# Performance work log

Measured on AMD Instinct MI355X. Metric: run time of the kernel, lower is better.

The kernel has to match this reference:

```python
import jax, jax.numpy as jnp
import numpy as np

E, D_IN, H1, H2 = 10, 784, 256, 64


def setup_inputs() -> dict:
    key = jax.random.key(0)
    ks = jax.random.split(key, 11)
    s = lambda fan_in: 1.0 / np.sqrt(fan_in)
    return {
        "x": jax.random.normal(ks[0], (65536, D_IN), dtype=jnp.float32),
        # stacked expert weights (E experts of Linear layers)
        "W1": jax.random.uniform(ks[1], (E, D_IN, H1), jnp.float32, -s(D_IN), s(D_IN)),
        "b1": jax.random.uniform(ks[2], (E, H1), jnp.float32, -s(D_IN), s(D_IN)),
        "W2": jax.random.uniform(ks[3], (E, H1, H2), jnp.float32, -s(H1), s(H1)),
        "b2": jax.random.uniform(ks[4], (E, H2), jnp.float32, -s(H1), s(H1)),
        "W3": jax.random.uniform(ks[5], (E, H2), jnp.float32, -s(H2), s(H2)),  # [E,64,1] squeezed
        "b3": jax.random.uniform(ks[6], (E,), jnp.float32, -s(H2), s(H2)),
        # gate: 784 -> 256 -> E
        "Wg1": jax.random.uniform(ks[7], (D_IN, H1), jnp.float32, -s(D_IN), s(D_IN)),
        "bg1": jax.random.uniform(ks[8], (H1,), jnp.float32, -s(D_IN), s(D_IN)),
        "Wg2": jax.random.uniform(ks[9], (H1, E), jnp.float32, -s(H1), s(H1)),
        "bg2": jax.random.uniform(ks[10], (E,), jnp.float32, -s(H1), s(H1)),
    }


def reference(x, W1, b1, W2, b2, W3, b3, Wg1, bg1, Wg2, bg2):
    # dense all-experts MLP stack, batched over experts as grouped GEMMs
    h = jax.nn.relu(jnp.einsum("bi,eih->beh", x, W1) + b1)        # [B,E,256]
    h = jax.nn.relu(jnp.einsum("beh,ehk->bek", h, W2) + b2)        # [B,E,64]
    expert_outputs = jnp.einsum("bek,ek->be", h, W3) + b3          # [B,E]
    g = jax.nn.relu(x @ Wg1 + bg1)
    gate_scores = jax.nn.softmax(g @ Wg2 + bg2, axis=-1)           # [B,E]
    output = gate_scores * expert_outputs                          # [B,E]
    return (output, gate_scores, expert_outputs)
```

## Files before the change

### kernel.cpp

```cpp
#include <hip/hip_runtime.h>
#include <hip/hip_bf16.h>
#include <stdint.h>

#define BTOT   65536
#define DIN    784
#define K1P    800
#define NH1    256
#define NH2    64
#define NEXP   10
#define BM     64
#define NKS1   25
#define NKS2   9

#define XS_B      102400
#define H_OFF     XS_B
#define H_B       36864
#define EXP2_OFF  (H_OFF + H_B)
#define W3S_OFF   (EXP2_OFF + BM * NEXP * 2 * 4)
#define B3S_OFF   (W3S_OFF + NEXP * NH2 * 4)
#define LDS_TOTAL (B3S_OFF + 64)

typedef short s16x8  __attribute__((ext_vector_type(8)));
typedef float f32x4  __attribute__((ext_vector_type(4)));
typedef float f32x16 __attribute__((ext_vector_type(16)));

__device__ __forceinline__ short bf16b(float v) {
    __bf16 b = (__bf16)v;
    return __builtin_bit_cast(short, b);
}

__global__ void prep_w1(const float* __restrict__ W1, const float* __restrict__ b1,
                        const float* __restrict__ Wg1, const float* __restrict__ bg1,
                        __bf16* __restrict__ dst) {
    int t = blockIdx.x * 256 + threadIdx.x;
    int lane = t & 63;
    int rr = t >> 6;
    int kh = rr & 1;
    int ks = (rr >> 1) % 25;
    int nb = ((rr >> 1) / 25) % 8;
    int e  = (rr >> 1) / 200;
    int n  = nb * 32 + (lane & 31);
    int k0 = ks * 32 + kh * 16 + (lane >> 5) * 8;
    const float* src  = (e < NEXP) ? (W1 + (size_t)e * DIN * NH1) : Wg1;
    const float* bias = (e < NEXP) ? (b1 + e * NH1) : bg1;
    s16x8 o;
    #pragma unroll
    for (int j = 0; j < 8; ++j) {
        int k = k0 + j;
        float v = (k < DIN) ? src[(size_t)k * NH1 + n]
                            : ((k == DIN) ? bias[n] : 0.f);
        o[j] = bf16b(v);
    }
    *(s16x8*)((short*)dst + (size_t)t * 8) = o;
}

__global__ void prep_w2(const float* __restrict__ W2, const float* __restrict__ b2,
                        __bf16* __restrict__ dst) {
    int t = blockIdx.x * 256 + threadIdx.x;
    int lane = t & 63;
    int rr = t >> 6;
    int kh = rr & 1;
    int ks = (rr >> 1) % 9;
    int jb = ((rr >> 1) / 9) & 1;
    int e  = (rr >> 1) / 18;
    int n  = jb * 32 + (lane & 31);
    int k0 = ks * 32 + kh * 16 + (lane >> 5) * 8;
    s16x8 o;
    #pragma unroll
    for (int j = 0; j < 8; ++j) {
        int k = k0 + j;
        float v = (k < NH1) ? W2[((size_t)e * NH1 + k) * NH2 + n]
                            : ((k == NH1) ? b2[e * NH2 + n] : 0.f);
        o[j] = bf16b(v);
    }
    *(s16x8*)((short*)dst + (size_t)t * 8) = o;
}

__global__ void prep_wg2(const float* __restrict__ Wg2, const float* __restrict__ bg2,
                         __bf16* __restrict__ dst) {
    int t = blockIdx.x * 256 + threadIdx.x;
    if (t >= 9 * 2 * 64) return;
    int lane = t & 63;
    int rr = t >> 6;
    int kh = rr & 1;
    int ks = rr >> 1;
    int n  = lane & 31;
    int k0 = ks * 32 + kh * 16 + (lane >> 5) * 8;
    s16x8 o;
    #pragma unroll
    for (int j = 0; j < 8; ++j) {
        int k = k0 + j;
        float v = 0.f;
        if (n < NEXP) {
            if (k < NH1)       v = Wg2[(size_t)k * NEXP + n];
            else if (k == NH1) v = bg2[n];
        }
        o[j] = bf16b(v);
    }
    *(s16x8*)((short*)dst + (size_t)t * 8) = o;
}

#define PFA(S, T)                                                             \
    { _Pragma("unroll") for (int mt = 0; mt < 2; ++mt)                        \
        _Pragma("unroll") for (int kh = 0; kh < 2; ++kh)                      \
            a[S][mt][kh] = *(const s16x8*)(pA + ((mt * 25 + (T)) * 2 + kh) * 1024); }

#define PFW(S, E, T, PW)                                                      \
    { _Pragma("unroll") for (int nt = 0; nt < 2; ++nt)                        \
        _Pragma("unroll") for (int kh = 0; kh < 2; ++kh)                      \
            w[S][E][nt][kh] = *(const s16x8*)((PW) + nt * 51200                \
                                              + ((T) * 2 + kh) * 1024); }

#define PMMA(S, E)                                                            \
    { _Pragma("unroll") for (int nt = 0; nt < 2; ++nt)                        \
        _Pragma("unroll") for (int mt = 0; mt < 2; ++mt)                      \
            _Pragma("unroll") for (int kh = 0; kh < 2; ++kh)                  \
                acc[E][nt][mt] = __builtin_amdgcn_mfma_f32_32x32x16_bf16(     \
                    w[S][E][nt][kh], a[S][mt][kh], acc[E][nt][mt], 0, 0, 0); }

#define ZACC(E)                                                               \
    { _Pragma("unroll") for (int nt = 0; nt < 2; ++nt)                        \
        _Pragma("unroll") for (int mt = 0; mt < 2; ++mt)                      \
            _Pragma("unroll") for (int q = 0; q < 16; ++q)                    \
                acc[E][nt][mt][q] = 0.f; }

#define HWRITE(E)                                                             \
    { _Pragma("unroll") for (int mt = 0; mt < 2; ++mt)                        \
        _Pragma("unroll") for (int nt = 0; nt < 2; ++nt) {                    \
            const int ks2 = wave * 2 + nt;                                    \
            _Pragma("unroll") for (int q = 0; q < 4; ++q) {                   \
                uint2 wv; short* p = (short*)&wv;                             \
                _Pragma("unroll") for (int r2 = 0; r2 < 4; ++r2)              \
                    p[r2] = bf16b(fmaxf(acc[E][nt][mt][q * 4 + r2], 0.f));    \
                *(uint2*)(hb + ((mt * 9 + ks2) * 2 + (q >> 1)) * 1024         \
                             + (q & 1) * 512 + rl * 16 + hi * 8) = wv;        \
            } } }

#define PF_V2(PV)                                                             \
    { _Pragma("unroll") for (int p = 0; p < 3; ++p)                           \
        _Pragma("unroll") for (int kh = 0; kh < 2; ++kh)                      \
            v2[p][kh] = *(const s16x8*)((PV) + (p * 2 + kh) * 1024); }

#define L2_PF(S, T)                                                           \
    { _Pragma("unroll") for (int kh = 0; kh < 2; ++kh) {                      \
        hfr[S][kh] = *(const s16x8*)(pH + ((T) * 2 + kh) * 1024);             \
        v2[S][kh]  = *(const s16x8*)(pV + ((T) * 2 + kh) * 1024); } }

#define L2_MMA(S)                                                             \
    { _Pragma("unroll") for (int kh = 0; kh < 2; ++kh)                        \
        acc2 = __builtin_amdgcn_mfma_f32_32x32x16_bf16(                       \
            v2[S][kh], hfr[S][kh], acc2, 0, 0, 0); }

#define DO_L2(EV, PV)                                                         \
    {                                                                         \
        const char* pV = (PV);                                                \
        f32x16 acc2;                                                          \
        _Pragma("unroll") for (int q = 0; q < 16; ++q) acc2[q] = 0.f;         \
        _Pragma("unroll") for (int kh = 0; kh < 2; ++kh)                      \
            hfr[0][kh] = *(const s16x8*)(pH + (0 * 2 + kh) * 1024);           \
        _Pragma("unroll") for (int kh = 0; kh < 2; ++kh)                      \
            hfr[1][kh] = *(const s16x8*)(pH + (1 * 2 + kh) * 1024);           \
        _Pragma("unroll") for (int kh = 0; kh < 2; ++kh)                      \
            hfr[2][kh] = *(const s16x8*)(pH + (2 * 2 + kh) * 1024);           \
        _Pragma("unroll 1") for (int T = 0; T < 2; ++T) {                     \
            const int t3 = 3 * T;                                             \
            L2_MMA(0) L2_PF(0, t3 + 3)                                        \
            L2_MMA(1) L2_PF(1, t3 + 4)                                        \
            L2_MMA(2) L2_PF(2, t3 + 5)                                        \
        }                                                                     \
        L2_MMA(0) L2_MMA(1) L2_MMA(2)                                         \
        float part = 0.f;                                                     \
        const float* w3p = w3s + (EV) * NH2 + jb * 32 + 4 * hi;               \
        _Pragma("unroll") for (int q = 0; q < 4; ++q) {                       \
            f32x4 w3v = *(const f32x4*)(w3p + 8 * q);                         \
            _Pragma("unroll") for (int r2 = 0; r2 < 4; ++r2)                  \
                part += fmaxf(acc2[q * 4 + r2], 0.f) * w3v[r2];               \
        }                                                                     \
        part += __shfl_xor(part, 32, 64);                                     \
        if (hi == 0)                                                          \
            expl2[(mb2 * 32 + rl) * (NEXP * 2) + (EV) * 2 + jb] = part;       \
    }

__global__ void __launch_bounds__(256, 1)
moe_fused(const float* __restrict__ x, const float* __restrict__ W3,
          const float* __restrict__ b3, const __bf16* __restrict__ w1t,
          const __bf16* __restrict__ w2t, const __bf16* __restrict__ wg2t,
          float* __restrict__ out)
{
    extern __shared__ char lds[];
    char*  xsb   = lds;
    char*  hb    = lds + H_OFF;
    float* expl2 = (float*)(lds + EXP2_OFF);
    float* w3s   = (float*)(lds + W3S_OFF);
    float* b3s   = (float*)(lds + B3S_OFF);

    const int tid  = threadIdx.x;
    const int lane = tid & 63;
    const int wave = tid >> 6;
    const int rl   = lane & 31;
    const int hi   = lane >> 5;
    const int row0 = blockIdx.x * BM;
    const char* w1c = (const char*)w1t;

    const char* pA = xsb + lane * 16;
    const int mb2 = wave >> 1, jb = wave & 1;
    const char* pH = hb + mb2 * 18432 + lane * 16;

    s16x8 w[2][2][2][2];
    s16x8 a[2][2][2];
    s16x8 v2[3][2], hfr[3][2];
    {
        const char* pW0 = w1c + (size_t)(wave * 2) * 51200 + lane * 16;
        const char* pW1 = pW0 + 8 * 51200;
        PFW(0, 0, 0, pW0) PFW(1, 0, 1, pW0)
        PFW(0, 1, 0, pW1) PFW(1, 1, 1, pW1)
    }

    {
        const float* xg = x + (size_t)row0 * DIN;
        #pragma unroll 4
        for (int i = 0; i < 49; ++i) {
            int idx = tid + i * 256;
            int r = idx / 196, c = (idx % 196) * 4;
            float4 v = *(const float4*)(xg + (size_t)r * DIN + c);
            int ks = c >> 5, kin = c & 31;
            int kh = kin >> 4, hw = (kin >> 3) & 1, j = c & 7;
            uint2 wv; short* p = (short*)&wv;
            p[0] = bf16b(v.x); p[1] = bf16b(v.y);
            p[2] = bf16b(v.z); p[3] = bf16b(v.w);
            *(uint2*)(xsb + ((((r >> 5) * 25 + ks) * 2 + kh) * 2 + hw) * 512
                          + (r & 31) * 16 + j * 2) = wv;
        }
        for (int i = tid; i < 64 * 4; i += 256) {
            int r = i >> 2, g = i & 3;
            int hw = g >> 1, j0 = (g & 1) * 4;
            uint2 wv = {0u, 0u};
            if (g == 0) ((short*)&wv)[0] = bf16b(1.f);
            *(uint2*)(xsb + ((((r >> 5) * 25 + 24) * 2 + 1) * 2 + hw) * 512
                          + (r & 31) * 16 + j0 * 2) = wv;
        }
        for (int i = tid; i < 2 * 1024; i += 256) {
            int mb = i >> 10, q = i & 1023;
            short v = (q < 256 && (q & 7) == 0) ? bf16b(1.f) : (short)0;
            *(short*)(hb + (mb * 9 + 8) * 2048 + q * 2) = v;
        }
        for (int i = tid; i < NEXP * NH2; i += 256) w3s[i] = W3[i];
        if (tid < NEXP) b3s[tid] = b3[tid];
    }
    __syncthreads();

    PFA(0, 0) PFA(1, 1)

    f32x16 acc[2][2][2];

    #pragma unroll 1
    for (int p5 = 0; p5 < 5; ++p5) {
        const int e0 = 2 * p5;
        const char* pW0 = w1c + (size_t)(e0 * 8 + wave * 2) * 51200 + lane * 16;
        const char* pW1 = pW0 + 8 * 51200;

        ZACC(0) ZACC(1)

        #pragma unroll 1
        for (int T = 0; T < 11; ++T) {
            const int t2 = 2 * T;
            PMMA(0, 0) PMMA(0, 1)
            PFW(0, 0, t2 + 2, pW0) PFW(0, 1, t2 + 2, pW1) PFA(0, t2 + 2)
            PMMA(1, 0) PMMA(1, 1)
            PFW(1, 0, t2 + 3, pW0) PFW(1, 1, t2 + 3, pW1) PFA(1, t2 + 3)
        }
        PMMA(0, 0) PMMA(0, 1)
        PFW(0, 0, 24, pW0) PFW(0, 1, 24, pW1) PFA(0, 24)
        PMMA(1, 0) PMMA(1, 1)
        PMMA(0, 0) PMMA(0, 1)

        PF_V2((const char*)w2t + (size_t)(e0 * 2 + jb) * 18432 + lane * 16)
        {
            const char* pW0n = pW0 + 16 * 51200;
            const char* pW1n = (p5 < 4) ? (pW1 + 16 * 51200) : pW0n;
            PFW(0, 0, 0, pW0n) PFW(1, 0, 1, pW0n)
            PFW(0, 1, 0, pW1n) PFW(1, 1, 1, pW1n)
            PFA(0, 0) PFA(1, 1)
        }

        __syncthreads();
        HWRITE(0)
        __syncthreads();
        DO_L2(e0, (const char*)w2t + (size_t)(e0 * 2 + jb) * 18432 + lane * 16)
        PF_V2((const char*)w2t + (size_t)((e0 + 1) * 2 + jb) * 18432 + lane * 16)
        __syncthreads();
        HWRITE(1)
        __syncthreads();
        DO_L2(e0 + 1, (const char*)w2t + (size_t)((e0 + 1) * 2 + jb) * 18432 + lane * 16)
    }

    {
        const char* pWg = w1c + (size_t)(10 * 8 + wave * 2) * 51200 + lane * 16;
        ZACC(0)
        #pragma unroll 1
        for (int T = 0; T < 11; ++T) {
            const int t2 = 2 * T;
            PMMA(0, 0) PFW(0, 0, t2 + 2, pWg) PFA(0, t2 + 2)
            PMMA(1, 0) PFW(1, 0, t2 + 3, pWg) PFA(1, t2 + 3)
        }
        PMMA(0, 0) PFW(0, 0, 24, pWg) PFA(0, 24)
        PMMA(1, 0)
        PMMA(0, 0)

        __syncthreads();
        HWRITE(0)
        __syncthreads();
    }

    if (wave < 2) {
        const int mbg = wave;
        const char* pHg = hb + mbg * 18432 + lane * 16;
        const char* pG  = (const char*)wg2t + lane * 16;
        f32x16 acc3;
        #pragma unroll
        for (int q = 0; q < 16; ++q) acc3[q] = 0.f;
        {
            const char* pH = pHg;
            const char* pV = pG;
            L2_PF(0, 0) L2_PF(1, 1) L2_PF(2, 2)
            #define acc2 acc3
            #pragma unroll 1
            for (int T = 0; T < 2; ++T) {
                const int t3 = 3 * T;
                L2_MMA(0) L2_PF(0, t3 + 3)
                L2_MMA(1) L2_PF(1, t3 + 4)
                L2_MMA(2) L2_PF(2, t3 + 5)
            }
            L2_MMA(0) L2_MMA(1) L2_MMA(2)
            #undef acc2
        }
        const int m = mbg * 32 + rl;
        float mx = -1e30f;
        float lv[16];
        #pragma unroll
        for (int q = 0; q < 4; ++q)
            #pragma unroll
            for (int r2 = 0; r2 < 4; ++r2) {
                int j = r2 + 8 * q + 4 * hi;
                int rg = q * 4 + r2;
                lv[rg] = (j < NEXP) ? acc3[rg] : -1e30f;
                mx = fmaxf(mx, lv[rg]);
            }
        mx = fmaxf(mx, __shfl_xor(mx, 32, 64));
        float s = 0.f;
        float pv[16];
        #pragma unroll
        for (int rg = 0; rg < 16; ++rg) {
            pv[rg] = (lv[rg] > -1e29f) ? __expf(lv[rg] - mx) : 0.f;
            s += pv[rg];
        }
        s += __shfl_xor(s, 32, 64);
        const float inv = 1.f / s;
        #pragma unroll
        for (int q = 0; q < 4; ++q)
            #pragma unroll
            for (int r2 = 0; r2 < 4; ++r2) {
                int j = r2 + 8 * q + 4 * hi;
                if (j < NEXP) {
                    float g  = pv[q * 4 + r2] * inv;
                    float eo = expl2[m * (NEXP * 2) + j * 2]
                             + expl2[m * (NEXP * 2) + j * 2 + 1]
                             + b3s[j];
                    size_t o = (size_t)(row0 + m) * NEXP + j;
                    out[o] = g * eo;
                    out[(size_t)BTOT * NEXP + o] = g;
                    out[(size_t)2 * BTOT * NEXP + o] = eo;
                }
            }
    }
}

extern "C" void kernel_launch(void* const* d_in, const int* in_sizes, int n_in,
                              void* d_out, int out_size, void* d_ws, size_t ws_size,
                              hipStream_t stream) {
    (void)in_sizes; (void)n_in; (void)out_size; (void)ws_size;
    const float* x   = (const float*)d_in[0];
    const float* W1  = (const float*)d_in[1];
    const float* b1  = (const float*)d_in[2];
    const float* W2  = (const float*)d_in[3];
    const float* b2  = (const float*)d_in[4];
    const float* W3  = (const float*)d_in[5];
    const float* b3  = (const float*)d_in[6];
    const float* Wg1 = (const float*)d_in[7];
    const float* bg1 = (const float*)d_in[8];
    const float* Wg2 = (const float*)d_in[9];
    const float* bg2 = (const float*)d_in[10];

    __bf16* w1t  = (__bf16*)d_ws;
    __bf16* w2t  = w1t + (size_t)11 * 8 * 25 * 2 * 64 * 8;
    __bf16* wg2t = w2t + (size_t)10 * 2 * 9 * 2 * 64 * 8;

    hipFuncSetAttribute((const void*)moe_fused,
                        hipFuncAttributeMaxDynamicSharedMemorySize, LDS_TOTAL);

    prep_w1<<<1100, 256, 0, stream>>>(W1, b1, Wg1, bg1, w1t);
    prep_w2<<<90, 256, 0, stream>>>(W2, b2, w2t);
    prep_wg2<<<5, 256, 0, stream>>>(Wg2, bg2, wg2t);
    moe_fused<<<BTOT / BM, 256, LDS_TOTAL, stream>>>(x, W3, b3, w1t, w2t, wg2t,
                                                     (float*)d_out);
}
```

Measured before the change: 354.2 us.

## Split work across 8 waves per block and dual-accumulate layer-2 MFMAs

```diff
diff --git a/kernel.cpp b/kernel.cpp
--- a/kernel.cpp
+++ b/kernel.cpp
@@ -100,41 +100,33 @@
     *(s16x8*)((short*)dst + (size_t)t * 8) = o;
 }
 
-#define PFA(S, T)                                                             \
+#define PFA8(S, T)                                                            \
     { _Pragma("unroll") for (int mt = 0; mt < 2; ++mt)                        \
         _Pragma("unroll") for (int kh = 0; kh < 2; ++kh)                      \
             a[S][mt][kh] = *(const s16x8*)(pA + ((mt * 25 + (T)) * 2 + kh) * 1024); }
 
-#define PFW(S, E, T, PW)                                                      \
-    { _Pragma("unroll") for (int nt = 0; nt < 2; ++nt)                        \
-        _Pragma("unroll") for (int kh = 0; kh < 2; ++kh)                      \
-            w[S][E][nt][kh] = *(const s16x8*)((PW) + nt * 51200                \
-                                              + ((T) * 2 + kh) * 1024); }
-
-#define PMMA(S, E)                                                            \
-    { _Pragma("unroll") for (int nt = 0; nt < 2; ++nt)                        \
+#define PFW8(S, E, T, PW)                                                     \
+    { _Pragma("unroll") for (int kh = 0; kh < 2; ++kh)                        \
+            w[S][E][kh] = *(const s16x8*)((PW) + ((T) * 2 + kh) * 1024); }
+
+#define PMMA8(S, E)                                                           \
+    { _Pragma("unroll") for (int kh = 0; kh < 2; ++kh)                        \
         _Pragma("unroll") for (int mt = 0; mt < 2; ++mt)                      \
-            _Pragma("unroll") for (int kh = 0; kh < 2; ++kh)                  \
-                acc[E][nt][mt] = __builtin_amdgcn_mfma_f32_32x32x16_bf16(     \
-                    w[S][E][nt][kh], a[S][mt][kh], acc[E][nt][mt], 0, 0, 0); }
-
-#define ZACC(E)                                                               \
-    { _Pragma("unroll") for (int nt = 0; nt < 2; ++nt)                        \
-        _Pragma("unroll") for (int mt = 0; mt < 2; ++mt)                      \
-            _Pragma("unroll") for (int q = 0; q < 16; ++q)                    \
-                acc[E][nt][mt][q] = 0.f; }
-
-#define HWRITE(E)                                                             \
+            acc[E][mt] = __builtin_amdgcn_mfma_f32_32x32x16_bf16(             \
+                w[S][E][kh], a[S][mt][kh], acc[E][mt], 0, 0, 0); }
+
+#define ZACC8(E)                                                              \
     { _Pragma("unroll") for (int mt = 0; mt < 2; ++mt)                        \
-        _Pragma("unroll") for (int nt = 0; nt < 2; ++nt) {                    \
-            const int ks2 = wave * 2 + nt;                                    \
-            _Pragma("unroll") for (int q = 0; q < 4; ++q) {                   \
-                uint2 wv; short* p = (short*)&wv;                             \
-                _Pragma("unroll") for (int r2 = 0; r2 < 4; ++r2)              \
-                    p[r2] = bf16b(fmaxf(acc[E][nt][mt][q * 4 + r2], 0.f));    \
-                *(uint2*)(hb + ((mt * 9 + ks2) * 2 + (q >> 1)) * 1024         \
-                             + (q & 1) * 512 + rl * 16 + hi * 8) = wv;        \
-            } } }
+        _Pragma("unroll") for (int q = 0; q < 16; ++q) acc[E][mt][q] = 0.f; }
+
+#define HWRITE8(E)                                                            \
+    { _Pragma("unroll") for (int mt = 0; mt < 2; ++mt)                        \
+        _Pragma("unroll") for (int q = 0; q < 4; ++q) {                       \
+            uint2 wv; short* p = (short*)&wv;                                 \
+            _Pragma("unroll") for (int r2 = 0; r2 < 4; ++r2)                  \
+                p[r2] = bf16b(fmaxf(acc[E][mt][q * 4 + r2], 0.f));            \
+            *(uint2*)(hb + ((mt * 9 + wave) * 2 + (q >> 1)) * 1024            \
+                         + (q & 1) * 512 + rl * 16 + hi * 8) = wv; } }
 
 #define PF_V2(PV)                                                             \
     { _Pragma("unroll") for (int p = 0; p < 3; ++p)                           \
@@ -147,15 +139,17 @@
         v2[S][kh]  = *(const s16x8*)(pV + ((T) * 2 + kh) * 1024); } }
 
 #define L2_MMA(S)                                                             \
-    { _Pragma("unroll") for (int kh = 0; kh < 2; ++kh)                        \
-        acc2 = __builtin_amdgcn_mfma_f32_32x32x16_bf16(                       \
-            v2[S][kh], hfr[S][kh], acc2, 0, 0, 0); }
+    { acc2a = __builtin_amdgcn_mfma_f32_32x32x16_bf16(v2[S][0], hfr[S][0],    \
+                                                      acc2a, 0, 0, 0);        \
+      acc2b = __builtin_amdgcn_mfma_f32_32x32x16_bf16(v2[S][1], hfr[S][1],    \
+                                                      acc2b, 0, 0, 0); }
 
 #define DO_L2(EV, PV)                                                         \
     {                                                                         \
         const char* pV = (PV);                                                \
-        f32x16 acc2;                                                          \
-        _Pragma("unroll") for (int q = 0; q < 16; ++q) acc2[q] = 0.f;         \
+        f32x16 acc2a, acc2b;                                                  \
+        _Pragma("unroll") for (int q = 0; q < 16; ++q) { acc2a[q] = 0.f;      \
+                                                         acc2b[q] = 0.f; }    \
         _Pragma("unroll") for (int kh = 0; kh < 2; ++kh)                      \
             hfr[0][kh] = *(const s16x8*)(pH + (0 * 2 + kh) * 1024);           \
         _Pragma("unroll") for (int kh = 0; kh < 2; ++kh)                      \
@@ -174,14 +168,15 @@
         _Pragma("unroll") for (int q = 0; q < 4; ++q) {                       \
             f32x4 w3v = *(const f32x4*)(w3p + 8 * q);                         \
             _Pragma("unroll") for (int r2 = 0; r2 < 4; ++r2)                  \
-                part += fmaxf(acc2[q * 4 + r2], 0.f) * w3v[r2];               \
+                part += fmaxf(acc2a[q * 4 + r2] + acc2b[q * 4 + r2], 0.f)     \
+                        * w3v[r2];                                            \
         }                                                                     \
         part += __shfl_xor(part, 32, 64);                                     \
         if (hi == 0)                                                          \
             expl2[(mb2 * 32 + rl) * (NEXP * 2) + (EV) * 2 + jb] = part;       \
     }
 
-__global__ void __launch_bounds__(256, 1)
+__global__ void __launch_bounds__(512, 2)
 moe_fused(const float* __restrict__ x, const float* __restrict__ W3,
           const float* __restrict__ b3, const __bf16* __restrict__ w1t,
           const __bf16* __restrict__ w2t, const __bf16* __restrict__ wg2t,
@@ -203,35 +198,37 @@
     const char* w1c = (const char*)w1t;
 
     const char* pA = xsb + lane * 16;
-    const int mb2 = wave >> 1, jb = wave & 1;
+    const int mb2 = (wave >> 2) & 1, jb = (wave >> 1) & 1;
     const char* pH = hb + mb2 * 18432 + lane * 16;
 
-    s16x8 w[2][2][2][2];
+    s16x8 w[2][2][2];
     s16x8 a[2][2][2];
     s16x8 v2[3][2], hfr[3][2];
     {
-        const char* pW0 = w1c + (size_t)(wave * 2) * 51200 + lane * 16;
+        const char* pW0 = w1c + (size_t)wave * 51200 + lane * 16;
         const char* pW1 = pW0 + 8 * 51200;
-        PFW(0, 0, 0, pW0) PFW(1, 0, 1, pW0)
-        PFW(0, 1, 0, pW1) PFW(1, 1, 1, pW1)
+        PFW8(0, 0, 0, pW0) PFW8(1, 0, 1, pW0)
+        PFW8(0, 1, 0, pW1) PFW8(1, 1, 1, pW1)
     }
 
     {
         const float* xg = x + (size_t)row0 * DIN;
-        #pragma unroll 4
-        for (int i = 0; i < 49; ++i) {
-            int idx = tid + i * 256;
-            int r = idx / 196, c = (idx % 196) * 4;
-            float4 v = *(const float4*)(xg + (size_t)r * DIN + c);
-            int ks = c >> 5, kin = c & 31;
-            int kh = kin >> 4, hw = (kin >> 3) & 1, j = c & 7;
-            uint2 wv; short* p = (short*)&wv;
-            p[0] = bf16b(v.x); p[1] = bf16b(v.y);
-            p[2] = bf16b(v.z); p[3] = bf16b(v.w);
-            *(uint2*)(xsb + ((((r >> 5) * 25 + ks) * 2 + kh) * 2 + hw) * 512
-                          + (r & 31) * 16 + j * 2) = wv;
-        }
-        for (int i = tid; i < 64 * 4; i += 256) {
+        #pragma unroll 2
+        for (int i = 0; i < 25; ++i) {
+            int idx = tid + i * 512;
+            if (idx < 12544) {
+                int r = idx / 196, c = (idx % 196) * 4;
+                float4 v = *(const float4*)(xg + (size_t)r * DIN + c);
+                int ks = c >> 5, kin = c & 31;
+                int kh = kin >> 4, hw = (kin >> 3) & 1;
+                uint2 wv; short* p = (short*)&wv;
+                p[0] = bf16b(v.x); p[1] = bf16b(v.y);
+                p[2] = bf16b(v.z); p[3] = bf16b(v.w);
+                *(uint2*)(xsb + ((((r >> 5) * 25 + ks) * 2 + kh) * 2 + hw) * 512
+                              + (r & 31) * 16 + (c & 7) * 2) = wv;
+            }
+        }
+        for (int i = tid; i < 64 * 4; i += 512) {
             int r = i >> 2, g = i & 3;
             int hw = g >> 1, j0 = (g & 1) * 4;
             uint2 wv = {0u, 0u};
@@ -239,91 +236,93 @@
             *(uint2*)(xsb + ((((r >> 5) * 25 + 24) * 2 + 1) * 2 + hw) * 512
                           + (r & 31) * 16 + j0 * 2) = wv;
         }
-        for (int i = tid; i < 2 * 1024; i += 256) {
+        for (int i = tid; i < 2 * 1024; i += 512) {
             int mb = i >> 10, q = i & 1023;
             short v = (q < 256 && (q & 7) == 0) ? bf16b(1.f) : (short)0;
             *(short*)(hb + (mb * 9 + 8) * 2048 + q * 2) = v;
         }
-        for (int i = tid; i < NEXP * NH2; i += 256) w3s[i] = W3[i];
+        for (int i = tid; i < NEXP * NH2; i += 512) w3s[i] = W3[i];
         if (tid < NEXP) b3s[tid] = b3[tid];
     }
     __syncthreads();
 
-    PFA(0, 0) PFA(1, 1)
-
-    f32x16 acc[2][2][2];
+    PFA8(0, 0) PFA8(1, 1)
+
+    f32x16 acc[2][2];
 
     #pragma unroll 1
     for (int p5 = 0; p5 < 5; ++p5) {
         const int e0 = 2 * p5;
-        const char* pW0 = w1c + (size_t)(e0 * 8 + wave * 2) * 51200 + lane * 16;
+        const char* pW0 = w1c + (size_t)(e0 * 8 + wave) * 51200 + lane * 16;
         const char* pW1 = pW0 + 8 * 51200;
 
-        ZACC(0) ZACC(1)
+        ZACC8(0) ZACC8(1)
 
         #pragma unroll 1
         for (int T = 0; T < 11; ++T) {
             const int t2 = 2 * T;
-            PMMA(0, 0) PMMA(0, 1)
-            PFW(0, 0, t2 + 2, pW0) PFW(0, 1, t2 + 2, pW1) PFA(0, t2 + 2)
-            PMMA(1, 0) PMMA(1, 1)
-            PFW(1, 0, t2 + 3, pW0) PFW(1, 1, t2 + 3, pW1) PFA(1, t2 + 3)
-        }
-        PMMA(0, 0) PMMA(0, 1)
-        PFW(0, 0, 24, pW0) PFW(0, 1, 24, pW1) PFA(0, 24)
-        PMMA(1, 0) PMMA(1, 1)
-        PMMA(0, 0) PMMA(0, 1)
-
+            PMMA8(0, 0) PMMA8(0, 1)
+            PFW8(0, 0, t2 + 2, pW0) PFW8(0, 1, t2 + 2, pW1) PFA8(0, t2 + 2)
+            PMMA8(1, 0) PMMA8(1, 1)
+            PFW8(1, 0, t2 + 3, pW0) PFW8(1, 1, t2 + 3, pW1) PFA8(1, t2 + 3)
+        }
+        PMMA8(0, 0) PMMA8(0, 1)
+        PFW8(0, 0, 24, pW0) PFW8(0, 1, 24, pW1) PFA8(0, 24)
+        PMMA8(1, 0) PMMA8(1, 1)
         PF_V2((const char*)w2t + (size_t)(e0 * 2 + jb) * 18432 + lane * 16)
+        PMMA8(0, 0) PMMA8(0, 1)
+
         {
             const char* pW0n = pW0 + 16 * 51200;
             const char* pW1n = (p5 < 4) ? (pW1 + 16 * 51200) : pW0n;
-            PFW(0, 0, 0, pW0n) PFW(1, 0, 1, pW0n)
-            PFW(0, 1, 0, pW1n) PFW(1, 1, 1, pW1n)
-            PFA(0, 0) PFA(1, 1)
-        }
-
-        __syncthreads();
-        HWRITE(0)
+            PFW8(0, 0, 0, pW0n) PFW8(1, 0, 1, pW0n)
+            PFW8(0, 1, 0, pW1n) PFW8(1, 1, 1, pW1n)
+            PFA8(0, 0) PFA8(1, 1)
+        }
+
+        __syncthreads();
+        HWRITE8(0)
         __syncthreads();
         DO_L2(e0, (const char*)w2t + (size_t)(e0 * 2 + jb) * 18432 + lane * 16)
         PF_V2((const char*)w2t + (size_t)((e0 + 1) * 2 + jb) * 18432 + lane * 16)
         __syncthreads();
-        HWRITE(1)
+        HWRITE8(1)
         __syncthreads();
         DO_L2(e0 + 1, (const char*)w2t + (size_t)((e0 + 1) * 2 + jb) * 18432 + lane * 16)
     }
 
     {
-        const char* pWg = w1c + (size_t)(10 * 8 + wave * 2) * 51200 + lane * 16;
-        ZACC(0)
+        const char* pWg = w1c + (size_t)(10 * 8 + wave) * 51200 + lane * 16;
+        ZACC8(0)
         #pragma unroll 1
         for (int T = 0; T < 11; ++T) {
             const int t2 = 2 * T;
-            PMMA(0, 0) PFW(0, 0, t2 + 2, pWg) PFA(0, t2 + 2)
-            PMMA(1, 0) PFW(1, 0, t2 + 3, pWg) PFA(1, t2 + 3)
-        }
-        PMMA(0, 0) PFW(0, 0, 24, pWg) PFA(0, 24)
-        PMMA(1, 0)
-        PMMA(0, 0)
-
-        __syncthreads();
-        HWRITE(0)
-        __syncthreads();
-    }
-
-    if (wave < 2) {
-        const int mbg = wave;
+            PMMA8(0, 0) PFW8(0, 0, t2 + 2, pWg) PFA8(0, t2 + 2)
+            PMMA8(1, 0) PFW8(1, 0, t2 + 3, pWg) PFA8(1, t2 + 3)
+        }
+        PMMA8(0, 0) PFW8(0, 0, 24, pWg) PFA8(0, 24)
+        PMMA8(1, 0)
+        PMMA8(0, 0)
+
+        __syncthreads();
+        HWRITE8(0)
+        __syncthreads();
+    }
+
+    {
+        const int mbg = wave >> 2;
         const char* pHg = hb + mbg * 18432 + lane * 16;
         const char* pG  = (const char*)wg2t + lane * 16;
-        f32x16 acc3;
+        f32x16 acc3a, acc3b;
         #pragma unroll
-        for (int q = 0; q < 16; ++q) acc3[q] = 0.f;
+        for (int q = 0; q < 16; ++q) { acc3a[q] = 0.f; acc3b[q] = 0.f; }
         {
+            s16x8 v2[3][2], hfr[3][2];
             const char* pH = pHg;
             const char* pV = pG;
             L2_PF(0, 0) L2_PF(1, 1) L2_PF(2, 2)
-            #define acc2 acc3
+            #define acc2a acc3a
+            #define acc2b acc3b
             #pragma unroll 1
             for (int T = 0; T < 2; ++T) {
                 const int t3 = 3 * T;
@@ -332,7 +331,8 @@
                 L2_MMA(2) L2_PF(2, t3 + 5)
             }
             L2_MMA(0) L2_MMA(1) L2_MMA(2)
-            #undef acc2
+            #undef acc2a
+            #undef acc2b
         }
         const int m = mbg * 32 + rl;
         float mx = -1e30f;
@@ -343,7 +343,7 @@
             for (int r2 = 0; r2 < 4; ++r2) {
                 int j = r2 + 8 * q + 4 * hi;
                 int rg = q * 4 + r2;
-                lv[rg] = (j < NEXP) ? acc3[rg] : -1e30f;
+                lv[rg] = (j < NEXP) ? (acc3a[rg] + acc3b[rg]) : -1e30f;
                 mx = fmaxf(mx, lv[rg]);
             }
         mx = fmaxf(mx, __shfl_xor(mx, 32, 64));
@@ -401,6 +401,6 @@
     prep_w1<<<1100, 256, 0, stream>>>(W1, b1, Wg1, bg1, w1t);
     prep_w2<<<90, 256, 0, stream>>>(W2, b2, w2t);
     prep_wg2<<<5, 256, 0, stream>>>(Wg2, bg2, wg2t);
-    moe_fused<<<BTOT / BM, 256, LDS_TOTAL, stream>>>(x, W3, b3, w1t, w2t, wg2t,
+    moe_fused<<<BTOT / BM, 512, LDS_TOTAL, stream>>>(x, W3, b3, w1t, w2t, wg2t,
                                                      (float*)d_out);
 }
```

Result: slower. 382.2 us (+7.9%).
